# Kernel optimization log

Measured on AMD Instinct MI355X. Metric: run time of the kernel, lower is better.

## Reference

```python
import jax, jax.numpy as jnp
import numpy as np

NEG = -100000000.0  # NOT_POSSIBLE_TRANSITION
B, T, F, NT = 64, 512, 1024, 50
H = NT + 2  # +2 for start/stop tags
START, STOP = H - 2, H - 1


def setup_inputs() -> dict:
    key = jax.random.key(0)
    k0, k1, k2, k3 = jax.random.split(key, 4)
    features = jax.random.normal(k0, (B, T, F), jnp.float32)
    tags = jax.random.randint(k1, (B, T), 0, NT)
    masks = jnp.ones((B, T), jnp.float32)
    W = jax.random.normal(k2, (H, F), jnp.float32) * 0.02  # nn.Linear weight
    b = jnp.zeros((H,), jnp.float32)                        # nn.Linear bias
    transition = jax.random.normal(k3, (H, H), jnp.float32)
    transition = transition.at[START, :].set(NEG).at[:, STOP].set(NEG)
    return dict(features=features, W=W, b=b, transition=transition,
                masks=masks, tags=tags)


def _forward_algorithm(emit, masks, transition):
    # emit: [B,T,H], masks: [B,T]
    b_, _, h = emit.shape
    init = jnp.full((b_, h), NEG, emit.dtype).at[:, START].set(0.0)

    def step(scores, xs):
        emit_t, mask_t = xs  # [B,H], [B]
        # score_t[b, i] = logsumexp_j(scores[b,j] + transition[i,j] + emit_t[b,i])
        s = scores[:, None, :] + transition[None, :, :] + emit_t[:, :, None]
        s = jax.nn.logsumexp(s, axis=-1)
        m = mask_t[:, None]
        scores = s * m + scores * (1.0 - m)
        return scores, None

    scores, _ = jax.lax.scan(step, init, (emit.transpose(1, 0, 2), masks.T))
    return jax.nn.logsumexp(scores + transition[STOP], axis=-1)  # [B]


def _gold_score(emit, tags, masks, transition):
    b_ = emit.shape[0]
    emit_sc = jnp.take_along_axis(emit, tags[:, :, None], axis=2)[:, :, 0]  # [B,T]
    start = jnp.full((b_, 1), START, tags.dtype)
    tags_ext = jnp.concatenate([start, tags], axis=1)  # [B,T+1]
    trans_sc = transition[tags_ext[:, 1:], tags_ext[:, :-1]]  # [B,T]
    last_pos = masks.sum(axis=1).astype(jnp.int32)  # index into tags_ext
    last_tag = jnp.take_along_axis(tags_ext, last_pos[:, None], axis=1)[:, 0]
    last_score = transition[STOP, last_tag]
    return ((trans_sc + emit_sc) * masks).sum(axis=1) + last_score  # [B]


def reference(features, W, b, transition, masks, tags):
    emit = features @ W.T + b  # [B,T,H]
    fwd = _forward_algorithm(emit, masks, transition)
    gold = _gold_score(emit, tags, masks, transition)
    return (fwd - gold).mean()  # CRF NLL loss (scalar)


if __name__ == "__main__":
    print(reference(**setup_inputs()))
```

## Files before the change

### kernel.cpp

```cpp
#include <hip/hip_runtime.h>
#include <hip/hip_bf16.h>
#include <math.h>


#define NEGV   (-100000000.0f)
#define BB     64
#define TT     512
#define FF     1024
#define HH     52
#define HP     64
#define S_START 50
#define S_STOP  51
#define NCH    16
#define CLEN   (TT / NCH)

typedef __bf16 bf16x8 __attribute__((ext_vector_type(8)));
typedef __bf16 bf16x4 __attribute__((ext_vector_type(4)));
typedef float  f32x4  __attribute__((ext_vector_type(4)));

#define WS_CHUNK  0u
#define WS_WBF    16777216u
#define WS_GOLD   16908288u
#define WS_CEXP   16908544u

__global__ __launch_bounds__(256) void k_prep(const float* __restrict__ W,
                                              __bf16* __restrict__ wbf,
                                              float* __restrict__ gold) {
  int n = blockIdx.x;
  if (n == 0 && threadIdx.x < BB) gold[threadIdx.x] = 0.0f;
  for (int k = threadIdx.x; k < FF; k += 256) {
    float v = (n < HH) ? W[n * FF + k] : 0.0f;
    wbf[n * FF + k] = (__bf16)v;
  }
}

__global__ __launch_bounds__(256, 1) void k_scan(const float* __restrict__ feat,
                                                 const __bf16* __restrict__ wbf,
                                                 const float* __restrict__ bias,
                                                 const float* __restrict__ trans,
                                                 const float* __restrict__ masks,
                                                 const int* __restrict__ tags,
                                                 float* __restrict__ chunks,
                                                 float* __restrict__ cexp,
                                                 float* __restrict__ gold) {
  const int tid = threadIdx.x;
  const int wv = tid >> 6;
  const int l  = tid & 63;
  const int lm = l & 15;
  const int q  = l >> 4;
  const int chunk = blockIdx.x * 4 + wv;
  const int b = chunk >> 4, c = chunk & 15;

  __shared__ __align__(16) __bf16 PTall[4][64 * 72];
  __shared__ __align__(16) float  Eall[4][CLEN * 64];
  __bf16* pt = PTall[wv];
  float*  el = Eall[wv];

  const float* fbase = feat + ((size_t)(b * TT + c * CLEN)) * FF;

  f32x4 apre[2][2][2];
#pragma unroll
  for (int s = 0; s < 2; ++s)
#pragma unroll
    for (int mt2 = 0; mt2 < 2; ++mt2)
#pragma unroll
      for (int h = 0; h < 2; ++h)
        apre[s][mt2][h] = *(const f32x4*)(fbase + (size_t)(mt2 * 16 + lm) * FF + s * 32 + q * 8 + h * 4);

  bf16x8 bcur[4];
#pragma unroll
  for (int nt = 0; nt < 4; ++nt)
    bcur[nt] = *(const bf16x8*)(wbf + (size_t)(nt * 16 + lm) * FF + q * 8);

  f32x4 acc[2][4] = {};

#pragma unroll
  for (int kt = 0; kt < 32; ++kt) {
    const int st = kt & 1;
    bf16x8 af[2];
#pragma unroll
    for (int mt2 = 0; mt2 < 2; ++mt2)
#pragma unroll
      for (int j = 0; j < 4; ++j) {
        af[mt2][j]     = (__bf16)apre[st][mt2][0][j];
        af[mt2][4 + j] = (__bf16)apre[st][mt2][1][j];
      }
    if (kt + 2 < 32) {
      const float* fa = fbase + (kt + 2) * 32 + q * 8;
#pragma unroll
      for (int mt2 = 0; mt2 < 2; ++mt2)
#pragma unroll
        for (int h = 0; h < 2; ++h)
          apre[st][mt2][h] = *(const f32x4*)(fa + (size_t)(mt2 * 16 + lm) * FF + h * 4);
    }
    bf16x8 bnx[4];
    if (kt + 1 < 32) {
#pragma unroll
      for (int nt = 0; nt < 4; ++nt)
        bnx[nt] = *(const bf16x8*)(wbf + (size_t)(nt * 16 + lm) * FF + (kt + 1) * 32 + q * 8);
    }
#pragma unroll
    for (int mt2 = 0; mt2 < 2; ++mt2)
#pragma unroll
      for (int nt = 0; nt < 4; ++nt)
        acc[mt2][nt] = __builtin_amdgcn_mfma_f32_16x16x32_bf16(af[mt2], bcur[nt], acc[mt2][nt], 0, 0, 0);
    if (kt + 1 < 32) {
#pragma unroll
      for (int nt = 0; nt < 4; ++nt) bcur[nt] = bnx[nt];
    }
  }

#pragma unroll
  for (int nt = 0; nt < 4; ++nt) {
    int n = nt * 16 + lm;
    float bn = (n < HH) ? bias[n] : 0.0f;
#pragma unroll
    for (int mt2 = 0; mt2 < 2; ++mt2)
#pragma unroll
      for (int rr = 0; rr < 4; ++rr)
        el[(mt2 * 16 + q * 4 + rr) * 64 + n] = acc[mt2][nt][rr] + bn;
  }

  float mreg = (l < CLEN) ? masks[b * TT + c * CLEN + l] : 1.0f;
  int cur = (l < CLEN) ? tags[b * TT + c * CLEN + l] : 0;
  int prev = __shfl_up(cur, 1);
  if (l == 0) prev = (c == 0) ? S_START : tags[b * TT + c * CLEN - 1];
  float gp = 0.0f;
  if (l < CLEN) {
    float e  = el[l * 64 + cur];
    float tr = trans[cur * HH + prev];
    gp = (e + tr) * mreg;
  }
#pragma unroll
  for (int d = 1; d < 64; d <<= 1) gp += __shfl_xor(gp, d);
  if (l == 0) atomicAdd(&gold[b], gp);

  bf16x8 afrag[4][2];
#pragma unroll
  for (int mt = 0; mt < 4; ++mt)
#pragma unroll
    for (int kk = 0; kk < 2; ++kk)
#pragma unroll
      for (int j = 0; j < 8; ++j) {
        int m = mt * 16 + lm, k = kk * 32 + q * 8 + j;
        float tv = (k >= HH) ? NEGV : ((m >= HH) ? 0.0f : trans[m * HH + k]);
        afrag[mt][kk][j] = (__bf16)__expf(tv);
      }

  for (int idx = l; idx < 4096; idx += 64) {
    int n = idx >> 6, mm = idx & 63;
    pt[n * 72 + mm] = (__bf16)((n == mm) ? 1.0f : 0.0f);
  }

  int eacc = 0, rpend = 0;
  const float LOG2E = 1.4426950408889634f;

  for (int t = 0; t < CLEN; ++t) {
    float mcur = __shfl(mreg, t);
    if (mcur != 0.0f) {
      float sh = (float)(7 + rpend);
      eacc += 7 + rpend;
      rpend = 0;
      float s[4][4];
#pragma unroll
      for (int mt = 0; mt < 4; ++mt) {
        f32x4 em = *(const f32x4*)&el[t * 64 + mt * 16 + q * 4];
#pragma unroll
        for (int rr = 0; rr < 4; ++rr)
          s[mt][rr] = __builtin_amdgcn_exp2f(fmaf(em[rr], LOG2E, -sh));
      }

      bf16x8 bfr[2][4];
#pragma unroll
      for (int kk = 0; kk < 2; ++kk)
#pragma unroll
        for (int nt = 0; nt < 4; ++nt)
          bfr[kk][nt] = *(const bf16x8*)&pt[(nt * 16 + lm) * 72 + kk * 32 + q * 8];

      const bool trk = ((t & 7) == 7) && (t != CLEN - 1);
      float lmax = 0.0f;
      f32x4 zero = {};
#pragma unroll
      for (int mt = 0; mt < 4; ++mt) {
#pragma unroll
        for (int nt = 0; nt < 4; ++nt) {
          f32x4 a = __builtin_amdgcn_mfma_f32_16x16x32_bf16(afrag[mt][0], bfr[0][nt], zero, 0, 0, 0);
          a = __builtin_amdgcn_mfma_f32_16x16x32_bf16(afrag[mt][1], bfr[1][nt], a, 0, 0, 0);
          bf16x4 w4;
#pragma unroll
          for (int rr = 0; rr < 4; ++rr) {
            float v = a[rr] * s[mt][rr];
            if (trk) lmax = fmaxf(lmax, v);
            w4[rr] = (__bf16)v;
          }
          *(bf16x4*)&pt[(nt * 16 + lm) * 72 + mt * 16 + q * 4] = w4;
        }
      }
      if (trk) {
#pragma unroll
        for (int d = 1; d < 64; d <<= 1) lmax = fmaxf(lmax, __shfl_xor(lmax, d));
        rpend = ilogbf(lmax);
      }
    }
  }

  for (int idx = l; idx < 4096; idx += 64) {
    int jj = idx >> 8, i = (idx >> 2) & 63, jr = idx & 3;
    chunks[(size_t)chunk * 4096 + idx] = (float)pt[(jj * 4 + jr) * 72 + i];
  }
  if (l == 0) cexp[chunk] = (float)eacc;
}

__global__ __launch_bounds__(64) void k_combine(const float* __restrict__ chunks,
                                                const float* __restrict__ cexp,
                                                const float* __restrict__ trans,
                                                const float* __restrict__ masks,
                                                const int* __restrict__ tags,
                                                const float* __restrict__ gold,
                                                float* __restrict__ out) {
  const int b = blockIdx.x;
  const int l = threadIdx.x;
  __shared__ float vsh[64];
  float v = (l == S_START) ? 1.0f : 0.0f;
  float esum = 0.0f;
  const float LN2 = 0.6931471805599453f;

  float msum = 0.0f;
  for (int t = l; t < TT; t += 64) msum += masks[b * TT + t];

  f32x4 mb[2][16];
  {
    const f32x4* M = (const f32x4*)(chunks + ((size_t)(b * NCH)) * 4096);
#pragma unroll
    for (int jj = 0; jj < 16; ++jj) mb[0][jj] = M[jj * 64 + l];
  }

#pragma unroll
  for (int cc = 0; cc < NCH; ++cc) {
    vsh[l] = v;
    __syncthreads();
    if (cc + 1 < NCH) {
      const f32x4* Mn = (const f32x4*)(chunks + ((size_t)(b * NCH + cc + 1)) * 4096);
#pragma unroll
      for (int jj = 0; jj < 16; ++jj) mb[(cc + 1) & 1][jj] = Mn[jj * 64 + l];
    }
    f32x4 u4 = {};
#pragma unroll
    for (int jj = 0; jj < 16; ++jj) {
      f32x4 m4 = mb[cc & 1][jj];
      const float* vj = &vsh[jj * 4];
      u4[0] += m4[0] * vj[0];
      u4[1] += m4[1] * vj[1];
      u4[2] += m4[2] * vj[2];
      u4[3] += m4[3] * vj[3];
    }
    float u = (u4[0] + u4[1]) + (u4[2] + u4[3]);
    esum += cexp[b * NCH + cc] * LN2;
    float mxx = u;
#pragma unroll
    for (int d = 1; d < 64; d <<= 1) mxx = fmaxf(mxx, __shfl_xor(mxx, d));
    if (mxx > 0.0f) {
      int ee = ilogbf(mxx);
      u = ldexpf(u, -ee);
      esum += (float)ee * LN2;
    }
    v = u;
    __syncthreads();
  }

  float ts = (l < HH) ? trans[S_STOP * HH + l] : NEGV;
  float contrib = v * __expf(ts);
#pragma unroll
  for (int d = 1; d < 64; d <<= 1) {
    contrib += __shfl_xor(contrib, d);
    msum += __shfl_xor(msum, d);
  }
  if (l == 0) {
    int lp = (int)(msum + 0.5f);
    int lt = (lp == 0) ? S_START : tags[b * TT + lp - 1];
    float goldb = gold[b] + trans[S_STOP * HH + lt];
    float fwd = __logf(contrib) + esum;
    atomicAdd(out, (fwd - goldb) * (1.0f / 64.0f));
  }
}

extern "C" void kernel_launch(void* const* d_in, const int* in_sizes, int n_in,
                              void* d_out, int out_size, void* d_ws, size_t ws_size,
                              hipStream_t stream) {
  (void)in_sizes; (void)n_in; (void)out_size; (void)ws_size;
  const float* feat  = (const float*)d_in[0];
  const float* W     = (const float*)d_in[1];
  const float* bias  = (const float*)d_in[2];
  const float* trans = (const float*)d_in[3];
  const float* masks = (const float*)d_in[4];
  const int*   tags  = (const int*)d_in[5];

  char* ws = (char*)d_ws;
  float*  chunks = (float*)(ws + WS_CHUNK);
  __bf16* wbf    = (__bf16*)(ws + WS_WBF);
  float*  gold   = (float*)(ws + WS_GOLD);
  float*  cexp   = (float*)(ws + WS_CEXP);

  hipMemsetAsync(d_out, 0, sizeof(float), stream);
  k_prep<<<HP, 256, 0, stream>>>(W, wbf, gold);
  k_scan<<<(BB * NCH) / 4, 256, 0, stream>>>(feat, wbf, bias, trans, masks, tags,
                                             chunks, cexp, gold);
  k_combine<<<BB, 64, 0, stream>>>(chunks, cexp, trans, masks, tags, gold, (float*)d_out);
}
```

Measured before the change: 270.5 us.

## Split scan into 32 chunks per sequence and precompute exp(transition) once

Doubles the number of time chunks per sequence, so each wave does a 16-step scan with a single M-tile GEMM and there are twice as many blocks, at occupancy 2. The exp(transition) matrix is now built once in the prep kernel and loaded as bf16, emissions are held in LDS as bf16, and chunk matrices are written back as vectorized float4 stores. This shortens the serial chain per wave and raises parallelism, but k_combine has to multiply twice as many 64x64 chunk matrices per batch, and the bf16 emissions lose precision.

Measured after the change: 262.5 us. -3.0%, faster.

```diff
diff --git a/kernel.cpp b/kernel.cpp
--- a/kernel.cpp
+++ b/kernel.cpp
@@ -11,7 +11,7 @@
 #define HP     64
 #define S_START 50
 #define S_STOP  51
-#define NCH    16
+#define NCH    32
 #define CLEN   (TT / NCH)
 
 typedef __bf16 bf16x8 __attribute__((ext_vector_type(8)));
@@ -19,23 +19,34 @@
 typedef float  f32x4  __attribute__((ext_vector_type(4)));
 
 #define WS_CHUNK  0u
-#define WS_WBF    16777216u
-#define WS_GOLD   16908288u
-#define WS_CEXP   16908544u
+#define WS_WBF    33554432u
+#define WS_EXPT   33685504u
+#define WS_GOLD   33693696u
+#define WS_CEXP   33693952u
 
 __global__ __launch_bounds__(256) void k_prep(const float* __restrict__ W,
+                                              const float* __restrict__ trans,
                                               __bf16* __restrict__ wbf,
+                                              __bf16* __restrict__ expT,
                                               float* __restrict__ gold) {
   int n = blockIdx.x;
-  if (n == 0 && threadIdx.x < BB) gold[threadIdx.x] = 0.0f;
+  if (n == 0) {
+    if (threadIdx.x < BB) gold[threadIdx.x] = 0.0f;
+    for (int idx = threadIdx.x; idx < 4096; idx += 256) {
+      int m = idx >> 6, k = idx & 63;
+      float tv = (k >= HH) ? NEGV : ((m >= HH) ? 0.0f : trans[m * HH + k]);
+      expT[idx] = (__bf16)__expf(tv);
+    }
+  }
   for (int k = threadIdx.x; k < FF; k += 256) {
     float v = (n < HH) ? W[n * FF + k] : 0.0f;
     wbf[n * FF + k] = (__bf16)v;
   }
 }
 
-__global__ __launch_bounds__(256, 1) void k_scan(const float* __restrict__ feat,
+__global__ __launch_bounds__(256, 2) void k_scan(const float* __restrict__ feat,
                                                  const __bf16* __restrict__ wbf,
+                                                 const __bf16* __restrict__ expT,
                                                  const float* __restrict__ bias,
                                                  const float* __restrict__ trans,
                                                  const float* __restrict__ masks,
@@ -49,49 +60,43 @@
   const int lm = l & 15;
   const int q  = l >> 4;
   const int chunk = blockIdx.x * 4 + wv;
-  const int b = chunk >> 4, c = chunk & 15;
+  const int b = chunk >> 5, c = chunk & 31;
 
   __shared__ __align__(16) __bf16 PTall[4][64 * 72];
-  __shared__ __align__(16) float  Eall[4][CLEN * 64];
+  __shared__ __align__(16) __bf16 Eall[4][CLEN * 64];
   __bf16* pt = PTall[wv];
-  float*  el = Eall[wv];
+  __bf16* el = Eall[wv];
 
   const float* fbase = feat + ((size_t)(b * TT + c * CLEN)) * FF;
-
-  f32x4 apre[2][2][2];
-#pragma unroll
-  for (int s = 0; s < 2; ++s)
-#pragma unroll
-    for (int mt2 = 0; mt2 < 2; ++mt2)
-#pragma unroll
-      for (int h = 0; h < 2; ++h)
-        apre[s][mt2][h] = *(const f32x4*)(fbase + (size_t)(mt2 * 16 + lm) * FF + s * 32 + q * 8 + h * 4);
+  const float* arow  = fbase + (size_t)lm * FF + q * 8;
+
+  f32x4 apre[4][2];
+#pragma unroll
+  for (int s = 0; s < 4; ++s)
+#pragma unroll
+    for (int h = 0; h < 2; ++h)
+      apre[s][h] = *(const f32x4*)(arow + s * 32 + h * 4);
 
   bf16x8 bcur[4];
 #pragma unroll
   for (int nt = 0; nt < 4; ++nt)
     bcur[nt] = *(const bf16x8*)(wbf + (size_t)(nt * 16 + lm) * FF + q * 8);
 
-  f32x4 acc[2][4] = {};
+  f32x4 acc[4] = {};
 
 #pragma unroll
   for (int kt = 0; kt < 32; ++kt) {
-    const int st = kt & 1;
-    bf16x8 af[2];
-#pragma unroll
-    for (int mt2 = 0; mt2 < 2; ++mt2)
-#pragma unroll
-      for (int j = 0; j < 4; ++j) {
-        af[mt2][j]     = (__bf16)apre[st][mt2][0][j];
-        af[mt2][4 + j] = (__bf16)apre[st][mt2][1][j];
-      }
-    if (kt + 2 < 32) {
-      const float* fa = fbase + (kt + 2) * 32 + q * 8;
-#pragma unroll
-      for (int mt2 = 0; mt2 < 2; ++mt2)
-#pragma unroll
-        for (int h = 0; h < 2; ++h)
-          apre[st][mt2][h] = *(const f32x4*)(fa + (size_t)(mt2 * 16 + lm) * FF + h * 4);
+    const int st = kt & 3;
+    bf16x8 af;
+#pragma unroll
+    for (int j = 0; j < 4; ++j) {
+      af[j]     = (__bf16)apre[st][0][j];
+      af[4 + j] = (__bf16)apre[st][1][j];
+    }
+    if (kt + 4 < 32) {
+#pragma unroll
+      for (int h = 0; h < 2; ++h)
+        apre[st][h] = *(const f32x4*)(arow + (kt + 4) * 32 + h * 4);
     }
     bf16x8 bnx[4];
     if (kt + 1 < 32) {
@@ -100,10 +105,8 @@
         bnx[nt] = *(const bf16x8*)(wbf + (size_t)(nt * 16 + lm) * FF + (kt + 1) * 32 + q * 8);
     }
 #pragma unroll
-    for (int mt2 = 0; mt2 < 2; ++mt2)
-#pragma unroll
-      for (int nt = 0; nt < 4; ++nt)
-        acc[mt2][nt] = __builtin_amdgcn_mfma_f32_16x16x32_bf16(af[mt2], bcur[nt], acc[mt2][nt], 0, 0, 0);
+    for (int nt = 0; nt < 4; ++nt)
+      acc[nt] = __builtin_amdgcn_mfma_f32_16x16x32_bf16(af, bcur[nt], acc[nt], 0, 0, 0);
     if (kt + 1 < 32) {
 #pragma unroll
       for (int nt = 0; nt < 4; ++nt) bcur[nt] = bnx[nt];
@@ -115,10 +118,8 @@
     int n = nt * 16 + lm;
     float bn = (n < HH) ? bias[n] : 0.0f;
 #pragma unroll
-    for (int mt2 = 0; mt2 < 2; ++mt2)
-#pragma unroll
-      for (int rr = 0; rr < 4; ++rr)
-        el[(mt2 * 16 + q * 4 + rr) * 64 + n] = acc[mt2][nt][rr] + bn;
+    for (int rr = 0; rr < 4; ++rr)
+      el[(q * 4 + rr) * 64 + n] = (__bf16)(acc[nt][rr] + bn);
   }
 
   float mreg = (l < CLEN) ? masks[b * TT + c * CLEN + l] : 1.0f;
@@ -127,7 +128,7 @@
   if (l == 0) prev = (c == 0) ? S_START : tags[b * TT + c * CLEN - 1];
   float gp = 0.0f;
   if (l < CLEN) {
-    float e  = el[l * 64 + cur];
+    float e  = (float)el[l * 64 + cur];
     float tr = trans[cur * HH + prev];
     gp = (e + tr) * mreg;
   }
@@ -140,12 +141,7 @@
   for (int mt = 0; mt < 4; ++mt)
 #pragma unroll
     for (int kk = 0; kk < 2; ++kk)
-#pragma unroll
-      for (int j = 0; j < 8; ++j) {
-        int m = mt * 16 + lm, k = kk * 32 + q * 8 + j;
-        float tv = (k >= HH) ? NEGV : ((m >= HH) ? 0.0f : trans[m * HH + k]);
-        afrag[mt][kk][j] = (__bf16)__expf(tv);
-      }
+      afrag[mt][kk] = *(const bf16x8*)&expT[(mt * 16 + lm) * 64 + kk * 32 + q * 8];
 
   for (int idx = l; idx < 4096; idx += 64) {
     int n = idx >> 6, mm = idx & 63;
@@ -164,10 +160,10 @@
       float s[4][4];
 #pragma unroll
       for (int mt = 0; mt < 4; ++mt) {
-        f32x4 em = *(const f32x4*)&el[t * 64 + mt * 16 + q * 4];
+        bf16x4 em4 = *(const bf16x4*)&el[t * 64 + mt * 16 + q * 4];
 #pragma unroll
         for (int rr = 0; rr < 4; ++rr)
-          s[mt][rr] = __builtin_amdgcn_exp2f(fmaf(em[rr], LOG2E, -sh));
+          s[mt][rr] = __builtin_amdgcn_exp2f(fmaf((float)em4[rr], LOG2E, -sh));
       }
 
       bf16x8 bfr[2][4];
@@ -204,9 +200,13 @@
     }
   }
 
-  for (int idx = l; idx < 4096; idx += 64) {
-    int jj = idx >> 8, i = (idx >> 2) & 63, jr = idx & 3;
-    chunks[(size_t)chunk * 4096 + idx] = (float)pt[(jj * 4 + jr) * 72 + i];
+  f32x4* c4 = (f32x4*)(chunks + (size_t)chunk * 4096);
+#pragma unroll
+  for (int it = 0; it < 16; ++it) {
+    f32x4 v;
+#pragma unroll
+    for (int jr = 0; jr < 4; ++jr) v[jr] = (float)pt[(it * 4 + jr) * 72 + l];
+    c4[it * 64 + l] = v;
   }
   if (l == 0) cexp[chunk] = (float)eacc;
 }
@@ -298,12 +298,13 @@
   char* ws = (char*)d_ws;
   float*  chunks = (float*)(ws + WS_CHUNK);
   __bf16* wbf    = (__bf16*)(ws + WS_WBF);
+  __bf16* expT   = (__bf16*)(ws + WS_EXPT);
   float*  gold   = (float*)(ws + WS_GOLD);
   float*  cexp   = (float*)(ws + WS_CEXP);
 
   hipMemsetAsync(d_out, 0, sizeof(float), stream);
-  k_prep<<<HP, 256, 0, stream>>>(W, wbf, gold);
-  k_scan<<<(BB * NCH) / 4, 256, 0, stream>>>(feat, wbf, bias, trans, masks, tags,
-                                             chunks, cexp, gold);
+  k_prep<<<HP, 256, 0, stream>>>(W, trans, wbf, expT, gold);
+  k_scan<<<(BB * NCH) / 4, 256, 0, stream>>>(feat, wbf, expT, bias, trans, masks,
+                                             tags, chunks, cexp, gold);
   k_combine<<<BB, 64, 0, stream>>>(chunks, cexp, trans, masks, tags, gold, (float*)d_out);
 }
```
